# Performance work log

Hardware: AMD Instinct MI355X
Metric: run time of the kernel (lower is better)

The kernel has to match this reference:

```python
import jax, jax.numpy as jnp
import numpy as np
import math

NUM_HEADS = 16

def setup_inputs() -> dict:
    key = jax.random.key(0)
    k1, k2, k3 = jax.random.split(key, 3)
    B, S, H = 8, 4096, 1024
    return {
        "query_hidden_states": jax.random.normal(k1, (B, S, H), dtype=jnp.float32),
        "key_hidden_states": jax.random.normal(k2, (B, S, H), dtype=jnp.float32),
        "value_hidden_states": jax.random.normal(k3, (B, S, H), dtype=jnp.float32),
        "attention_mask": jnp.zeros((B, 1, 1, S), dtype=jnp.float32),
    }

def reference(query_hidden_states, key_hidden_states, value_hidden_states, attention_mask):
    # PuriAttention forward with defaults: query_att=False, key_att=False, multi_head=True.
    # The torch code computes full [B,h,S,S] scores then keeps only query row 0 (CLS);
    # mathematically identical to computing only the CLS query row, done here.
    B, S, H = query_hidden_states.shape
    nh = NUM_HEADS
    hd = H // nh
    # in-place: attention_mask[:, :, :, 0] -= 10000  (masks out key position 0)
    mask = attention_mask.at[:, :, :, 0].add(-10000.0)  # [B,1,1,S]
    q_cls = query_hidden_states[:, 0, :].reshape(B, nh, hd)          # [B,h,d]
    k = key_hidden_states.reshape(B, S, nh, hd)                       # [B,S,h,d]
    v = value_hidden_states.reshape(B, S, nh, hd)                     # [B,S,h,d]
    scores = jnp.einsum('bhd,bshd->bhs', q_cls, k) / math.sqrt(hd)    # [B,h,S]
    scores = scores + mask[:, 0, :, :]                                # broadcast [B,1,S]
    probs = jax.nn.softmax(scores, axis=-1)                           # [B,h,S]
    ctx = jnp.einsum('bhs,bshd->bhd', probs, v)                       # [B,h,d]
    attention_output = ctx.reshape(B, 1, H)                           # [B,1,all_head]
    # permuted cls_info tensors: [B,1,h,S]
    scores_out = scores[:, None, :, :]
    probs_out = probs[:, None, :, :]
    return attention_output, scores_out, probs_out
```

## Files before the change

### kernel.cpp

```cpp
#include <hip/hip_runtime.h>

#define B    8
#define S    4096
#define H    1024
#define NH   16
#define HD   64
#define HALF 2048
#define NW   16
#define MAGICHI 0x5117C0DEu

typedef unsigned long long ull;

__device__ __forceinline__ ull packf(float v) {
    return ((ull)MAGICHI << 32) | (ull)__float_as_uint(v);
}
__device__ __forceinline__ float spin_read(ull* slot) {
    ull vv;
    do { vv = atomicAdd(slot, 0ull); } while ((unsigned)(vv >> 32) != MAGICHI);
    return __uint_as_float((unsigned)vv);
}

__global__ __launch_bounds__(1024)
void fused_attn(const float* __restrict__ q,
                const float* __restrict__ k,
                const float* __restrict__ v,
                const float* __restrict__ mask,
                float* __restrict__ ctx,
                float* __restrict__ scores,
                float* __restrict__ probs,
                ull* __restrict__ ws) {
    __shared__ float  sarr[HALF];
    __shared__ float  pexp[HALF];
    __shared__ float  wsum[NW];
    __shared__ float4 wred[NW][16];
    __shared__ float4 ctxown4[16];
    __shared__ float  esh[2];

    const int bid  = blockIdx.x;
    const int row  = bid >> 1;
    const int half = bid & 1;
    const int b = row >> 4;
    const int h = row & 15;
    const int t = threadIdx.x;
    const int w = t >> 6;
    const int l = t & 63;
    const int g = l >> 4;
    const int c = l & 15;
    const int sbase = half * HALF;

    ull* slotE = ws + (size_t)row * 80;
    ull* slotC = slotE + 16;

    const float4 qv = *(const float4*)(q + (size_t)b * S * H + h * HD + c * 4);
    const float* kb = k + (size_t)b * S * H + h * HD + c * 4;
    const float* mb = mask + b * S;

    float esum = 0.f;
#pragma unroll 4
    for (int i = 0; i < HALF / (NW * 4); ++i) {
        const int sl = i * (NW * 4) + w * 4 + g;
        const int s  = sbase + sl;
        const float4 kv = *(const float4*)(kb + (size_t)s * H);
        float d = kv.x * qv.x + kv.y * qv.y + kv.z * qv.z + kv.w * qv.w;
        d += __shfl_xor(d, 1); d += __shfl_xor(d, 2);
        d += __shfl_xor(d, 4); d += __shfl_xor(d, 8);
        const float sc = d * 0.125f + mb[s] + (s == 0 ? -10000.0f : 0.0f);
        const float e  = __expf(sc);
        if (c == 0) { sarr[sl] = sc; pexp[sl] = e; }
        esum += e;
    }
    esum += __shfl_xor(esum, 16);
    esum += __shfl_xor(esum, 32);
    if (l == 0) wsum[w] = esum;
    __syncthreads();

    if (t == 0) {
        float es = 0.f;
#pragma unroll
        for (int i = 0; i < NW; ++i) es += wsum[i];
        esh[0] = es;
        atomicExch(&slotE[half], packf(es));
    }

    {
        float* so = scores + (size_t)row * S + sbase;
        so[t]        = sarr[t];
        so[t + 1024] = sarr[t + 1024];
    }

    const float* vb = v + (size_t)b * S * H + h * HD + c * 4;
    float4 acc = {0.f, 0.f, 0.f, 0.f};
#pragma unroll 4
    for (int i = 0; i < HALF / (NW * 4); ++i) {
        const int sl = i * (NW * 4) + w * 4 + g;
        const int s  = sbase + sl;
        const float4 vv = *(const float4*)(vb + (size_t)s * H);
        const float p  = pexp[sl];
        acc.x += p * vv.x; acc.y += p * vv.y;
        acc.z += p * vv.z; acc.w += p * vv.w;
    }
    acc.x += __shfl_xor(acc.x, 16); acc.y += __shfl_xor(acc.y, 16);
    acc.z += __shfl_xor(acc.z, 16); acc.w += __shfl_xor(acc.w, 16);
    acc.x += __shfl_xor(acc.x, 32); acc.y += __shfl_xor(acc.y, 32);
    acc.z += __shfl_xor(acc.z, 32); acc.w += __shfl_xor(acc.w, 32);
    if (l < 16) wred[w][l] = acc;
    __syncthreads();

    if (t < 16) {
        float4 a = wred[0][t];
#pragma unroll
        for (int i = 1; i < NW; ++i) {
            const float4 x = wred[i][t];
            a.x += x.x; a.y += x.y; a.z += x.z; a.w += x.w;
        }
        ctxown4[t] = a;
    }
    __syncthreads();

    const float* cf = (const float*)ctxown4;
    float* po = probs + (size_t)row * S + sbase;

    if (half == 1) {
        if (t < HD) atomicExch(&slotC[t], packf(cf[t]));
        if (t == 0) esh[1] = spin_read(&slotE[0]);
        __syncthreads();
        const float inv = 1.0f / (esh[0] + esh[1]);
        po[t]        = pexp[t] * inv;
        po[t + 1024] = pexp[t + 1024] * inv;
    } else {
        if (t == 0) esh[1] = spin_read(&slotE[1]);
        __syncthreads();
        const float inv = 1.0f / (esh[0] + esh[1]);
        po[t]        = pexp[t] * inv;
        po[t + 1024] = pexp[t + 1024] * inv;
        if (t < HD) {
            const float pf = spin_read(&slotC[t]);
            ctx[(size_t)row * HD + t] = (cf[t] + pf) * inv;
        }
    }
}

extern "C" void kernel_launch(void* const* d_in, const int* in_sizes, int n_in,
                              void* d_out, int out_size, void* d_ws, size_t ws_size,
                              hipStream_t stream) {
    const float* q    = (const float*)d_in[0];
    const float* k    = (const float*)d_in[1];
    const float* v    = (const float*)d_in[2];
    const float* mask = (const float*)d_in[3];

    float* out    = (float*)d_out;
    float* ctx    = out;
    float* scores = out + B * H;
    float* probs  = out + B * H + B * NH * S;

    fused_attn<<<dim3(B * NH * 2), dim3(1024), 0, stream>>>(
        q, k, v, mask, ctx, scores, probs, (ull*)d_ws);
}
```

Baseline: 45.98 us.

## Split each attention row across four blocks and fuse K and V passes

Each (batch, head) row is now split across four workgroups instead of two, giving 512 blocks so more of the GPU's compute units are busy. The separate score and value loops are merged into one loop that loads K and V together and accumulates exp-weighted V on the fly, which removes the second pass and the intermediate LDS reads. Partial sums and context vectors are exchanged through spin-waited workspace slots. This relies on all four blocks of a row being co-resident, so it carries a deadlock risk, and it adds more cross-block synchronisation traffic.

```diff
diff --git a/kernel.cpp b/kernel.cpp
--- a/kernel.cpp
+++ b/kernel.cpp
@@ -5,7 +5,8 @@
 #define H    1024
 #define NH   16
 #define HD   64
-#define HALF 2048
+#define NSPLIT 4
+#define SPL  (S / NSPLIT)
 #define NW   16
 #define MAGICHI 0x5117C0DEu
 
@@ -20,7 +21,7 @@
     return __uint_as_float((unsigned)vv);
 }
 
-__global__ __launch_bounds__(1024)
+__global__ __launch_bounds__(1024, 8)
 void fused_attn(const float* __restrict__ q,
                 const float* __restrict__ k,
                 const float* __restrict__ v,
@@ -29,16 +30,16 @@
                 float* __restrict__ scores,
                 float* __restrict__ probs,
                 ull* __restrict__ ws) {
-    __shared__ float  sarr[HALF];
-    __shared__ float  pexp[HALF];
+    __shared__ float  sarr[SPL];
+    __shared__ float  pexp[SPL];
     __shared__ float  wsum[NW];
     __shared__ float4 wred[NW][16];
     __shared__ float4 ctxown4[16];
-    __shared__ float  esh[2];
+    __shared__ float  etot;
 
-    const int bid  = blockIdx.x;
-    const int row  = bid >> 1;
-    const int half = bid & 1;
+    const int bid   = blockIdx.x;
+    const int row   = bid >> 2;
+    const int split = bid & (NSPLIT - 1);
     const int b = row >> 4;
     const int h = row & 15;
     const int t = threadIdx.x;
@@ -46,59 +47,48 @@
     const int l = t & 63;
     const int g = l >> 4;
     const int c = l & 15;
-    const int sbase = half * HALF;
+    const int sbase = split * SPL;
 
-    ull* slotE = ws + (size_t)row * 80;
+    ull* slotE = ws + (size_t)row * 256;
     ull* slotC = slotE + 16;
 
     const float4 qv = *(const float4*)(q + (size_t)b * S * H + h * HD + c * 4);
     const float* kb = k + (size_t)b * S * H + h * HD + c * 4;
+    const float* vb = v + (size_t)b * S * H + h * HD + c * 4;
     const float* mb = mask + b * S;
 
-    float esum = 0.f;
-#pragma unroll 4
-    for (int i = 0; i < HALF / (NW * 4); ++i) {
-        const int sl = i * (NW * 4) + w * 4 + g;
-        const int s  = sbase + sl;
-        const float4 kv = *(const float4*)(kb + (size_t)s * H);
-        float d = kv.x * qv.x + kv.y * qv.y + kv.z * qv.z + kv.w * qv.w;
-        d += __shfl_xor(d, 1); d += __shfl_xor(d, 2);
-        d += __shfl_xor(d, 4); d += __shfl_xor(d, 8);
-        const float sc = d * 0.125f + mb[s] + (s == 0 ? -10000.0f : 0.0f);
-        const float e  = __expf(sc);
-        if (c == 0) { sarr[sl] = sc; pexp[sl] = e; }
-        esum += e;
+    float  esum = 0.f;
+    float4 acc  = {0.f, 0.f, 0.f, 0.f};
+    for (int i0 = 0; i0 < SPL / (NW * 4); i0 += 2) {
+        float4 kv[2], vv[2];
+        float  mm[2];
+#pragma unroll
+        for (int u = 0; u < 2; ++u) {
+            const int sl = (i0 + u) * (NW * 4) + w * 4 + g;
+            const int s  = sbase + sl;
+            kv[u] = *(const float4*)(kb + (size_t)s * H);
+            vv[u] = *(const float4*)(vb + (size_t)s * H);
+            mm[u] = mb[s];
+        }
+#pragma unroll
+        for (int u = 0; u < 2; ++u) {
+            const int sl = (i0 + u) * (NW * 4) + w * 4 + g;
+            const int s  = sbase + sl;
+            float d = kv[u].x * qv.x + kv[u].y * qv.y
+                    + kv[u].z * qv.z + kv[u].w * qv.w;
+            d += __shfl_xor(d, 1); d += __shfl_xor(d, 2);
+            d += __shfl_xor(d, 4); d += __shfl_xor(d, 8);
+            const float sc = d * 0.125f + mm[u] + (s == 0 ? -10000.0f : 0.0f);
+            const float e  = __expf(sc);
+            if (c == 0) { sarr[sl] = sc; pexp[sl] = e; }
+            esum += e;
+            acc.x += e * vv[u].x; acc.y += e * vv[u].y;
+            acc.z += e * vv[u].z; acc.w += e * vv[u].w;
+        }
     }
     esum += __shfl_xor(esum, 16);
     esum += __shfl_xor(esum, 32);
     if (l == 0) wsum[w] = esum;
-    __syncthreads();
-
-    if (t == 0) {
-        float es = 0.f;
-#pragma unroll
-        for (int i = 0; i < NW; ++i) es += wsum[i];
-        esh[0] = es;
-        atomicExch(&slotE[half], packf(es));
-    }
-
-    {
-        float* so = scores + (size_t)row * S + sbase;
-        so[t]        = sarr[t];
-        so[t + 1024] = sarr[t + 1024];
-    }
-
-    const float* vb = v + (size_t)b * S * H + h * HD + c * 4;
-    float4 acc = {0.f, 0.f, 0.f, 0.f};
-#pragma unroll 4
-    for (int i = 0; i < HALF / (NW * 4); ++i) {
-        const int sl = i * (NW * 4) + w * 4 + g;
-        const int s  = sbase + sl;
-        const float4 vv = *(const float4*)(vb + (size_t)s * H);
-        const float p  = pexp[sl];
-        acc.x += p * vv.x; acc.y += p * vv.y;
-        acc.z += p * vv.z; acc.w += p * vv.w;
-    }
     acc.x += __shfl_xor(acc.x, 16); acc.y += __shfl_xor(acc.y, 16);
     acc.z += __shfl_xor(acc.z, 16); acc.w += __shfl_xor(acc.w, 16);
     acc.x += __shfl_xor(acc.x, 32); acc.y += __shfl_xor(acc.y, 32);
@@ -106,6 +96,12 @@
     if (l < 16) wred[w][l] = acc;
     __syncthreads();
 
+    if (t == 0) {
+        float es = 0.f;
+#pragma unroll
+        for (int i = 0; i < NW; ++i) es += wsum[i];
+        atomicExch(&slotE[split], packf(es));
+    }
     if (t < 16) {
         float4 a = wred[0][t];
 #pragma unroll
@@ -115,28 +111,29 @@
         }
         ctxown4[t] = a;
     }
+    scores[(size_t)row * S + sbase + t] = sarr[t];
     __syncthreads();
 
     const float* cf = (const float*)ctxown4;
-    float* po = probs + (size_t)row * S + sbase;
+    if (split != 0 && t < HD)
+        atomicExch(&slotC[(size_t)(split - 1) * HD + t], packf(cf[t]));
+    if (t == 0) {
+        float es = 0.f;
+#pragma unroll
+        for (int sp = 0; sp < NSPLIT; ++sp)
+            es += spin_read(&slotE[sp]);
+        etot = es;
+    }
+    __syncthreads();
 
-    if (half == 1) {
-        if (t < HD) atomicExch(&slotC[t], packf(cf[t]));
-        if (t == 0) esh[1] = spin_read(&slotE[0]);
-        __syncthreads();
-        const float inv = 1.0f / (esh[0] + esh[1]);
-        po[t]        = pexp[t] * inv;
-        po[t + 1024] = pexp[t + 1024] * inv;
-    } else {
-        if (t == 0) esh[1] = spin_read(&slotE[1]);
-        __syncthreads();
-        const float inv = 1.0f / (esh[0] + esh[1]);
-        po[t]        = pexp[t] * inv;
-        po[t + 1024] = pexp[t + 1024] * inv;
-        if (t < HD) {
-            const float pf = spin_read(&slotC[t]);
-            ctx[(size_t)row * HD + t] = (cf[t] + pf) * inv;
-        }
+    const float inv = 1.0f / etot;
+    probs[(size_t)row * S + sbase + t] = pexp[t] * inv;
+    if (split == 0 && t < HD) {
+        float a = cf[t];
+#pragma unroll
+        for (int sp = 0; sp < NSPLIT - 1; ++sp)
+            a += spin_read(&slotC[(size_t)sp * HD + t]);
+        ctx[(size_t)row * HD + t] = a * inv;
     }
 }
 
@@ -153,6 +150,6 @@
     float* scores = out + B * H;
     float* probs  = out + B * H + B * NH * S;
 
-    fused_attn<<<dim3(B * NH * 2), dim3(1024), 0, stream>>>(
+    fused_attn<<<dim3(B * NH * NSPLIT), dim3(1024), 0, stream>>>(
         q, k, v, mask, ctx, scores, probs, (ull*)d_ws);
 }
```

Measured after the change: 88.72 us. +92.9%, slower.
